# Kernel tuning notes

Measured on AMD Instinct MI355X. Metric: run time of the kernel, lower is better.

Reference implementation:

```python
import jax, jax.numpy as jnp
import numpy as np
import math

N_ENTITIES = 200000
N_ITEMS = 100000
N_REL = 40
DIM = 64
N_HEADS = 2
DK = DIM // N_HEADS
N_EDGES = 1500000
K_EDGES = 256
K_ITEMS = 100


def setup_inputs() -> dict:
    key = jax.random.key(0)
    k1, k2, k3, k4, k5, k6 = jax.random.split(key, 6)
    entity_emb = jax.random.normal(k1, (N_ENTITIES, DIM), jnp.float32) * 0.1
    W_Q = jax.random.normal(k2, (DIM, DIM), jnp.float32) * (1.0 / math.sqrt(DIM))
    relation_emb = jax.random.normal(k3, (N_REL - 1, DIM), jnp.float32) * 0.1
    edge_index = jax.random.randint(k4, (2, N_EDGES), 0, N_ENTITIES, jnp.int32)
    # edge_type in [1, N_REL-1]: code indexes relation_emb[edge_type - 1]
    edge_type = jax.random.randint(k5, (N_EDGES,), 1, N_REL, jnp.int32)
    # uniform(0,1) driving the gumbel noise -log(-log(u)); clipped away from 0
    noise_u = jax.random.uniform(k6, (N_EDGES,), jnp.float32, 1e-9, 1.0)
    return {"entity_emb": entity_emb, "W_Q": W_Q, "relation_emb": relation_emb,
            "noise_u": noise_u, "edge_index": edge_index, "edge_type": edge_type}


def reference(entity_emb, W_Q, relation_emb, noise_u, edge_index, edge_type):
    head, tail = edge_index[0], edge_index[1]
    E = edge_index.shape[1]

    # --- norm_attn_computer (AttnHGCN): per-edge multi-head attention ---
    # project once on nodes, then gather (same math as (emb[head] @ W_Q))
    proj = entity_emb @ W_Q                               # [N, D]
    q = proj[head].reshape(E, N_HEADS, DK)                # [E, H, Dk]
    k = proj[tail].reshape(E, N_HEADS, DK)                # [E, H, Dk]
    rel = relation_emb[edge_type - 1].reshape(E, N_HEADS, DK)
    attn = jnp.sum(q * k * rel, axis=-1) / math.sqrt(DK)  # [E, H]
    edge_attn_logits = attn.mean(axis=-1)                 # [E]

    # scatter_softmax over head nodes, then multiply by head degree (norm)
    seg_max = jax.lax.stop_gradient(
        jax.ops.segment_max(edge_attn_logits, head, num_segments=N_ENTITIES))
    ex = jnp.exp(edge_attn_logits - seg_max[head])
    denom = jax.ops.segment_sum(ex, head, num_segments=N_ENTITIES)
    edge_attn_score = ex / denom[head]
    deg = jax.ops.segment_sum(jnp.ones_like(edge_attn_logits), head,
                              num_segments=N_ENTITIES)
    edge_attn_score = edge_attn_score * deg[head]         # [E]

    # --- attn logit sums per item (head + tail scatter_sum), topk 100 ---
    sum_by_node = (jax.ops.segment_sum(edge_attn_logits, head, num_segments=N_ENTITIES)
                   + jax.ops.segment_sum(edge_attn_logits, tail, num_segments=N_ENTITIES))
    top_items_v, top_attn_items = jax.lax.top_k(sum_by_node[:N_ITEMS], K_ITEMS)

    # --- gumbel-noise injection + edge topk 256 ---
    noisy_score = edge_attn_score + (-jnp.log(-jnp.log(noise_u)))
    topk_v, topk_attn_edge_id = jax.lax.top_k(noisy_score, K_EDGES)

    return (edge_attn_score, topk_v, topk_attn_edge_id, top_items_v, top_attn_items)
```

## Files before the change

kernel.cpp:

```cpp
#include <hip/hip_runtime.h>

#define N_ENTITIES 200000
#define N_ITEMS    100000
#define DIM        64
#define N_EDGES    1500000
#define K_EDGES    256
#define K_ITEMS    100
#define SCALE      0.08838834764831845f

#define CAND_CAP   4096
#define NSCANB     ((N_ENTITIES + 255) / 256)

typedef unsigned long long u64;

__device__ __forceinline__ unsigned fkey(float x) {
    unsigned u = __float_as_uint(x);
    return (u & 0x80000000u) ? ~u : (u | 0x80000000u);
}
__device__ __forceinline__ float funkey(unsigned k) {
    return (k & 0x80000000u) ? __uint_as_float(k & 0x7fffffffu)
                             : __uint_as_float(~k);
}

__device__ __forceinline__ void lds_hist_add(unsigned* h, unsigned bin, bool valid, int lane) {
    bool need = valid;
    for (;;) {
        unsigned long long mask = __ballot(need);
        if (mask == 0ull) break;
        int leader = __ffsll(mask) - 1;
        unsigned lbin = __shfl(bin, leader, 64);
        bool same = need && (bin == lbin);
        unsigned long long grp = __ballot(same);
        if (lane == leader) atomicAdd(&h[lbin], (unsigned)__popcll(grp));
        need = need && !same;
    }
}

__device__ __forceinline__ unsigned select_digit(const unsigned* __restrict__ hist,
                                                 unsigned Keff, unsigned* above) {
    unsigned cum = 0;
    int b = 255;
    for (; b > 0; --b) {
        unsigned hb = hist[b];
        if (cum + hb >= Keff) break;
        cum += hb;
    }
    *above = cum;
    return (unsigned)b;
}

__global__ __launch_bounds__(256) void proj_kernel(const float* __restrict__ emb,
                                                   const float* __restrict__ W,
                                                   float* __restrict__ proj,
                                                   const int* __restrict__ head,
                                                   unsigned* __restrict__ degi,
                                                   unsigned* __restrict__ rank) {
    int e = blockIdx.x * blockDim.x + threadIdx.x;
    if (e < N_EDGES) rank[e] = atomicAdd(&degi[head[e]], 1u);

    __shared__ float part[4][16][64];
    const int t = threadIdx.x;
    const int c = t & 63;
    const int q = __builtin_amdgcn_readfirstlane(t >> 6);

    float Wreg[16];
#pragma unroll
    for (int j = 0; j < 16; ++j) Wreg[j] = W[(q * 16 + j) * 64 + c];

    const int base = blockIdx.x * 16;
    const float* erow = emb + (size_t)base * 64 + q * 16;

    float acc[16];
#pragma unroll
    for (int r = 0; r < 16; ++r) acc[r] = 0.f;
#pragma unroll
    for (int r = 0; r < 16; ++r) {
#pragma unroll
        for (int j = 0; j < 16; ++j)
            acc[r] += erow[r * 64 + j] * Wreg[j];
    }
#pragma unroll
    for (int r = 0; r < 16; ++r) part[q][r][c] = acc[r];
    __syncthreads();
#pragma unroll
    for (int it = 0; it < 4; ++it) {
        int oi = t + it * 256;
        int r = oi >> 6, cc = oi & 63;
        float s = part[0][r][cc] + part[1][r][cc] + part[2][r][cc] + part[3][r][cc];
        proj[(size_t)(base + r) * 64 + cc] = s;
    }
}

__global__ void scan1_kernel(const unsigned* __restrict__ degi, unsigned* __restrict__ start,
                             unsigned* __restrict__ bsum) {
    __shared__ unsigned s[256];
    int t = threadIdx.x, i = blockIdx.x * 256 + t;
    unsigned v = (i < N_ENTITIES) ? degi[i] : 0u;
    s[t] = v;
    __syncthreads();
    for (int off = 1; off < 256; off <<= 1) {
        unsigned x = s[t];
        unsigned y = (t >= off) ? s[t - off] : 0u;
        __syncthreads();
        s[t] = x + y;
        __syncthreads();
    }
    if (i < N_ENTITIES) start[i] = s[t] - v;
    if (t == 255) bsum[blockIdx.x] = s[t];
}

__global__ __launch_bounds__(256) void scan23_kernel(const unsigned* __restrict__ bsum,
                                                     unsigned* __restrict__ start) {
    __shared__ unsigned part[4];
    const int b = blockIdx.x;
    const int t = threadIdx.x;
    unsigned s = 0;
    for (int j = t; j < b; j += 256) s += bsum[j];
#pragma unroll
    for (int off = 1; off < 64; off <<= 1) s += __shfl_xor(s, off, 64);
    if ((t & 63) == 0) part[t >> 6] = s;
    __syncthreads();
    unsigned prefix = part[0] + part[1] + part[2] + part[3];
    int i = b * 256 + t;
    if (i < N_ENTITIES) start[i] += prefix;
}

__global__ void scatter_kernel(const int* __restrict__ head, const int* __restrict__ tail,
                               const int* __restrict__ etype,
                               const unsigned* __restrict__ rank,
                               const unsigned* __restrict__ start,
                               u64* __restrict__ rec) {
    int i = blockIdx.x * blockDim.x + threadIdx.x;
    if (i >= N_EDGES) return;
    unsigned slot = start[head[i]] + rank[i];
    u64 R = ((u64)(unsigned)tail[i] << 27) | ((u64)(unsigned)(etype[i] - 1) << 21) | (u64)(unsigned)i;
    rec[slot] = R;
}

__global__ __launch_bounds__(256) void node_pass(const float4* __restrict__ proj4,
                                                 const float4* __restrict__ rel4,
                                                 const u64* __restrict__ rec,
                                                 const unsigned* __restrict__ start,
                                                 const unsigned* __restrict__ degi,
                                                 float* __restrict__ logits,
                                                 float2* __restrict__ nd,
                                                 float* __restrict__ sumhead,
                                                 float* __restrict__ sumtail) {
    int wave = (blockIdx.x * blockDim.x + threadIdx.x) >> 6;
    int lane = threadIdx.x & 63;
    int slot = lane >> 4, sl = lane & 15;
    unsigned s = start[wave], len = degi[wave];
    float4 ph = proj4[(size_t)wave * 16 + sl];
    float dsum = 0.f, lsum = 0.f;
    for (unsigned k0 = 0; k0 < len; k0 += 8) {
        unsigned ka = k0 + slot, kb = ka + 4;
        bool va = (ka < len), vb = (kb < len);
        u64 Ra = rec[s + (va ? ka : 0u)];
        u64 Rb = rec[s + (vb ? kb : 0u)];
        unsigned ta = (unsigned)(Ra >> 27), ra = ((unsigned)(Ra >> 21)) & 63u;
        unsigned tb = (unsigned)(Rb >> 27), rb = ((unsigned)(Rb >> 21)) & 63u;
        unsigned ea = (unsigned)Ra & 0x1FFFFFu, eb = (unsigned)Rb & 0x1FFFFFu;
        float4 pa = proj4[(size_t)ta * 16 + sl];
        float4 qa = rel4[(size_t)ra * 16 + sl];
        float4 pb = proj4[(size_t)tb * 16 + sl];
        float4 qb = rel4[(size_t)rb * 16 + sl];
        float xa = ph.x * pa.x * qa.x + ph.y * pa.y * qa.y + ph.z * pa.z * qa.z + ph.w * pa.w * qa.w;
        float xb = ph.x * pb.x * qb.x + ph.y * pb.y * qb.y + ph.z * pb.z * qb.z + ph.w * pb.w * qb.w;
        xa += __shfl_xor(xa, 1, 64);  xb += __shfl_xor(xb, 1, 64);
        xa += __shfl_xor(xa, 2, 64);  xb += __shfl_xor(xb, 2, 64);
        xa += __shfl_xor(xa, 4, 64);  xb += __shfl_xor(xb, 4, 64);
        xa += __shfl_xor(xa, 8, 64);  xb += __shfl_xor(xb, 8, 64);
        if (sl == 0) {
            if (va) {
                float lg = xa * SCALE;
                logits[ea] = lg;
                dsum += __expf(lg);
                lsum += lg;
                if (ta < N_ITEMS) atomicAdd(&sumtail[ta], lg);
            }
            if (vb) {
                float lg = xb * SCALE;
                logits[eb] = lg;
                dsum += __expf(lg);
                lsum += lg;
                if (tb < N_ITEMS) atomicAdd(&sumtail[tb], lg);
            }
        }
    }
    dsum += __shfl_xor(dsum, 16, 64);
    dsum += __shfl_xor(dsum, 32, 64);
    lsum += __shfl_xor(lsum, 16, 64);
    lsum += __shfl_xor(lsum, 32, 64);
    if (lane == 0) {
        nd[wave] = make_float2(dsum, (float)len);
        sumhead[wave] = lsum;
    }
}

__global__ void edge_pass3(const float* __restrict__ logits, const int* __restrict__ head,
                           const float2* __restrict__ nd, const float* __restrict__ noise_u,
                           const float* __restrict__ sumhead, const float* __restrict__ sumtail,
                           float* __restrict__ out_scores, unsigned* __restrict__ keysE,
                           unsigned* __restrict__ keysI, unsigned* __restrict__ hists) {
    __shared__ unsigned hE[256];
    __shared__ unsigned hI[256];
    for (int j = threadIdx.x; j < 256; j += blockDim.x) { hE[j] = 0; hI[j] = 0; }
    __syncthreads();
    int i = blockIdx.x * blockDim.x + threadIdx.x;
    int lane = threadIdx.x & 63;

    unsigned bin = 0;
    bool valid = (i < N_EDGES);
    if (valid) {
        float lg = logits[i];
        float2 dd = nd[head[i]];
        float score = __expf(lg) / dd.x * dd.y;
        out_scores[i] = score;
        float noise = -logf(-logf(noise_u[i]));
        unsigned k = fkey(score + noise);
        keysE[i] = k;
        bin = k >> 24;
    }
    lds_hist_add(hE, bin, valid, lane);

    bin = 0;
    valid = (i < N_ITEMS);
    if (valid) {
        float s = sumhead[i] + sumtail[i];
        unsigned k = fkey(s);
        keysI[i] = k;
        bin = k >> 24;
    }
    lds_hist_add(hI, bin, valid, lane);

    __syncthreads();
    for (int j = threadIdx.x; j < 256; j += blockDim.x) {
        unsigned v = hE[j];
        if (v) atomicAdd(&hists[j], v);
        v = hI[j];
        if (v) atomicAdd(&hists[3 * 256 + j], v);
    }
}

__global__ void hist_stage_kernel(const unsigned* __restrict__ keysE,
                                  const unsigned* __restrict__ keysI,
                                  unsigned* __restrict__ hists, int stage) {
    __shared__ unsigned h[256];
    for (int j = threadIdx.x; j < 256; j += blockDim.x) h[j] = 0;
    __syncthreads();
    const int y = blockIdx.y;
    const unsigned* keys = y ? keysI : keysE;
    const int n = y ? N_ITEMS : N_EDGES;
    const unsigned K = y ? K_ITEMS : K_EDGES;
    unsigned* H = hists + (size_t)y * 3 * 256;

    unsigned aboveA, prefix;
    unsigned binA = select_digit(H, K, &aboveA);
    if (stage == 1) {
        prefix = binA;
    } else {
        unsigned aboveB;
        unsigned binB = select_digit(H + 256, K - aboveA, &aboveB);
        prefix = (binA << 8) | binB;
    }
    const int shift = 24 - 8 * stage;
    unsigned* out = H + stage * 256;

    const int lane = threadIdx.x & 63;
    const int stride = gridDim.x * blockDim.x;
    for (int idx = blockIdx.x * blockDim.x + threadIdx.x; idx - lane < n; idx += stride) {
        bool valid = (idx < n);
        unsigned bin = 0;
        if (valid) {
            unsigned k = keys[idx];
            if ((k >> (shift + 8)) != prefix) valid = false;
            bin = (k >> shift) & 0xFFu;
        }
        lds_hist_add(h, bin, valid, lane);
    }
    __syncthreads();
    for (int j = threadIdx.x; j < 256; j += blockDim.x) {
        unsigned v = h[j];
        if (v) atomicAdd(&out[j], v);
    }
}

__global__ void collect_kernel(const unsigned* __restrict__ keysE,
                               const unsigned* __restrict__ keysI,
                               const unsigned* __restrict__ hists,
                               unsigned* __restrict__ counters, unsigned* __restrict__ cand) {
    const int y = blockIdx.y;
    const unsigned* keys = y ? keysI : keysE;
    const int n = y ? N_ITEMS : N_EDGES;
    const unsigned K = y ? K_ITEMS : K_EDGES;
    const unsigned* H = hists + (size_t)y * 3 * 256;
    unsigned aboveA, aboveB, aboveC;
    unsigned binA = select_digit(H, K, &aboveA);
    unsigned binB = select_digit(H + 256, K - aboveA, &aboveB);
    unsigned binC = select_digit(H + 512, K - aboveA - aboveB, &aboveC);
    const unsigned T = ((binA << 16) | (binB << 8) | binC) << 8;
    unsigned* cd = cand + (size_t)y * 2 * CAND_CAP;

    int i = blockIdx.x * blockDim.x + threadIdx.x;
    int stride = gridDim.x * blockDim.x;
    for (; i < n; i += stride) {
        unsigned k = keys[i];
        if (k >= T) {
            unsigned p = atomicAdd(&counters[y], 1u);
            if (p < (unsigned)CAND_CAP) { cd[2 * p] = k; cd[2 * p + 1] = (unsigned)i; }
        }
    }
}

__global__ void final_topk_kernel(const unsigned* __restrict__ cand,
                                  const unsigned* __restrict__ counters,
                                  float* __restrict__ out_topkv, float* __restrict__ out_topki,
                                  float* __restrict__ out_itemv, float* __restrict__ out_itemi) {
    __shared__ unsigned sk[CAND_CAP];
    __shared__ unsigned si[CAND_CAP];
    const int y = blockIdx.x;
    const int K = y ? K_ITEMS : K_EDGES;
    float* outv = y ? out_itemv : out_topkv;
    float* outi = y ? out_itemi : out_topki;
    const unsigned* cd = cand + (size_t)y * 2 * CAND_CAP;
    unsigned m = counters[y];
    if (m > (unsigned)CAND_CAP) m = CAND_CAP;
    for (unsigned i = threadIdx.x; i < m; i += blockDim.x) {
        sk[i] = cd[2 * i];
        si[i] = cd[2 * i + 1];
    }
    __syncthreads();
    for (unsigned i = threadIdx.x; i < m; i += blockDim.x) {
        unsigned ki = sk[i], xi = si[i];
        int r = 0;
        for (unsigned j = 0; j < m; ++j) {
            unsigned kj = sk[j];
            if (kj > ki || (kj == ki && si[j] < xi)) r++;
        }
        if (r < K) {
            outv[r] = funkey(ki);
            outi[r] = (float)xi;
        }
    }
}

extern "C" void kernel_launch(void* const* d_in, const int* in_sizes, int n_in,
                              void* d_out, int out_size, void* d_ws, size_t ws_size,
                              hipStream_t stream) {
    (void)in_sizes; (void)n_in; (void)out_size; (void)ws_size;
    const float* emb    = (const float*)d_in[0];
    const float* W      = (const float*)d_in[1];
    const float* rel    = (const float*)d_in[2];
    const float* noise  = (const float*)d_in[3];
    const int*   eidx   = (const int*)d_in[4];
    const int*   etype  = (const int*)d_in[5];
    const int* head = eidx;
    const int* tail = eidx + N_EDGES;

    float* out        = (float*)d_out;
    float* out_scores = out;
    float* out_topkv  = out + N_EDGES;
    float* out_topki  = out + N_EDGES + K_EDGES;
    float* out_itemv  = out + N_EDGES + 2 * K_EDGES;
    float* out_itemi  = out + N_EDGES + 2 * K_EDGES + K_ITEMS;

    float* ws = (float*)d_ws;
    size_t o = 0;
    float*    proj    = ws + o;               o += (size_t)N_ENTITIES * DIM;
    unsigned* rank    = (unsigned*)(ws + o);
    float*    logits  = ws + o;               o += N_EDGES;
    u64*      rec     = (u64*)(ws + o);       o += 2 * (size_t)N_EDGES;
    unsigned* keysE   = (unsigned*)rec;
    unsigned* keysI   = keysE + N_EDGES;
    unsigned* start   = (unsigned*)(ws + o);  o += N_ENTITIES;
    unsigned* degi    = (unsigned*)(ws + o);  o += N_ENTITIES;
    float*    sumtail = ws + o;               o += N_ITEMS;
    unsigned* hists   = (unsigned*)(ws + o);  o += 2 * 3 * 256;
    unsigned* counters= (unsigned*)(ws + o);  o += 2;
    float2*   nd      = (float2*)(ws + o);    o += 2 * (size_t)N_ENTITIES;
    float*    sumhead = ws + o;               o += N_ENTITIES;
    unsigned* bsum    = (unsigned*)(ws + o);  o += 1024;
    unsigned* cand    = (unsigned*)(ws + o);  o += 2 * 2 * CAND_CAP;

    hipMemsetAsync(degi, 0, (size_t)(N_ENTITIES + N_ITEMS + 2 * 3 * 256 + 2) * 4, stream);
    hipLaunchKernelGGL(proj_kernel, dim3(12500), dim3(256), 0, stream,
                       emb, W, proj, head, degi, rank);
    hipLaunchKernelGGL(scan1_kernel, dim3(NSCANB), dim3(256), 0, stream, degi, start, bsum);
    hipLaunchKernelGGL(scan23_kernel, dim3(NSCANB), dim3(256), 0, stream, bsum, start);
    hipLaunchKernelGGL(scatter_kernel, dim3((N_EDGES + 255) / 256), dim3(256), 0, stream,
                       head, tail, etype, rank, start, rec);
    hipLaunchKernelGGL(node_pass, dim3(N_ENTITIES / 4), dim3(256), 0, stream,
                       (const float4*)proj, (const float4*)rel, rec, start, degi,
                       logits, nd, sumhead, sumtail);
    hipLaunchKernelGGL(edge_pass3, dim3((N_EDGES + 255) / 256), dim3(256), 0, stream,
                       logits, head, (const float2*)nd, noise, sumhead, sumtail,
                       out_scores, keysE, keysI, hists);
    hipLaunchKernelGGL(hist_stage_kernel, dim3(512, 2), dim3(256), 0, stream,
                       keysE, keysI, hists, 1);
    hipLaunchKernelGGL(hist_stage_kernel, dim3(512, 2), dim3(256), 0, stream,
                       keysE, keysI, hists, 2);
    hipLaunchKernelGGL(collect_kernel, dim3(512, 2), dim3(256), 0, stream,
                       keysE, keysI, hists, counters, cand);
    hipLaunchKernelGGL(final_topk_kernel, dim3(2), dim3(1024), 0, stream,
                       cand, counters, out_topkv, out_topki, out_itemv, out_itemi);
}
```

Baseline: 502.3 us.

## Replicate tail-sum accumulators per XCD and defer rank store in projection

```diff
diff --git a/kernel.cpp b/kernel.cpp
--- a/kernel.cpp
+++ b/kernel.cpp
@@ -56,7 +56,9 @@
                                                    unsigned* __restrict__ degi,
                                                    unsigned* __restrict__ rank) {
     int e = blockIdx.x * blockDim.x + threadIdx.x;
-    if (e < N_EDGES) rank[e] = atomicAdd(&degi[head[e]], 1u);
+    unsigned rk = 0;
+    bool haveEdge = (e < N_EDGES);
+    if (haveEdge) rk = atomicAdd(&degi[head[e]], 1u);
 
     __shared__ float part[4][16][64];
     const int t = threadIdx.x;
@@ -89,6 +91,7 @@
         float s = part[0][r][cc] + part[1][r][cc] + part[2][r][cc] + part[3][r][cc];
         proj[(size_t)(base + r) * 64 + cc] = s;
     }
+    if (haveEdge) rank[e] = rk;
 }
 
 __global__ void scan1_kernel(const unsigned* __restrict__ degi, unsigned* __restrict__ start,
@@ -145,7 +148,12 @@
                                                  float* __restrict__ logits,
                                                  float2* __restrict__ nd,
                                                  float* __restrict__ sumhead,
-                                                 float* __restrict__ sumtail) {
+                                                 float* __restrict__ sumtailR,
+                                                 int repMask) {
+    unsigned xcd;
+    asm volatile("s_getreg_b32 %0, hwreg(HW_REG_XCC_ID)" : "=s"(xcd));
+    float* st = sumtailR + (size_t)(xcd & (unsigned)repMask) * N_ITEMS;
+
     int wave = (blockIdx.x * blockDim.x + threadIdx.x) >> 6;
     int lane = threadIdx.x & 63;
     int slot = lane >> 4, sl = lane & 15;
@@ -176,14 +184,14 @@
                 logits[ea] = lg;
                 dsum += __expf(lg);
                 lsum += lg;
-                if (ta < N_ITEMS) atomicAdd(&sumtail[ta], lg);
+                if (ta < N_ITEMS) atomicAdd(&st[ta], lg);
             }
             if (vb) {
                 float lg = xb * SCALE;
                 logits[eb] = lg;
                 dsum += __expf(lg);
                 lsum += lg;
-                if (tb < N_ITEMS) atomicAdd(&sumtail[tb], lg);
+                if (tb < N_ITEMS) atomicAdd(&st[tb], lg);
             }
         }
     }
@@ -199,7 +207,8 @@
 
 __global__ void edge_pass3(const float* __restrict__ logits, const int* __restrict__ head,
                            const float2* __restrict__ nd, const float* __restrict__ noise_u,
-                           const float* __restrict__ sumhead, const float* __restrict__ sumtail,
+                           const float* __restrict__ sumhead, const float* __restrict__ sumtailR,
+                           int R,
                            float* __restrict__ out_scores, unsigned* __restrict__ keysE,
                            unsigned* __restrict__ keysI, unsigned* __restrict__ hists) {
     __shared__ unsigned hE[256];
@@ -226,7 +235,8 @@
     bin = 0;
     valid = (i < N_ITEMS);
     if (valid) {
-        float s = sumhead[i] + sumtail[i];
+        float s = sumhead[i];
+        for (int r = 0; r < R; ++r) s += sumtailR[(size_t)r * N_ITEMS + i];
         unsigned k = fkey(s);
         keysI[i] = k;
         bin = k >> 24;
@@ -347,7 +357,7 @@
 extern "C" void kernel_launch(void* const* d_in, const int* in_sizes, int n_in,
                               void* d_out, int out_size, void* d_ws, size_t ws_size,
                               hipStream_t stream) {
-    (void)in_sizes; (void)n_in; (void)out_size; (void)ws_size;
+    (void)in_sizes; (void)n_in; (void)out_size;
     const float* emb    = (const float*)d_in[0];
     const float* W      = (const float*)d_in[1];
     const float* rel    = (const float*)d_in[2];
@@ -363,6 +373,15 @@
     float* out_topki  = out + N_EDGES + K_EDGES;
     float* out_itemv  = out + N_EDGES + 2 * K_EDGES;
     float* out_itemi  = out + N_EDGES + 2 * K_EDGES + K_ITEMS;
+
+    auto layout_floats = [](int R) -> size_t {
+        return (size_t)N_ENTITIES * DIM + N_EDGES + 2 * (size_t)N_EDGES
+             + N_ENTITIES + N_ENTITIES + (size_t)R * N_ITEMS
+             + 2 * 3 * 256 + 2 + 2 * (size_t)N_ENTITIES + N_ENTITIES
+             + 1024 + 2 * 2 * CAND_CAP;
+    };
+    int R = 8;
+    while (R > 1 && ws_size < layout_floats(R) * 4) R >>= 1;
 
     float* ws = (float*)d_ws;
     size_t o = 0;
@@ -374,7 +393,7 @@
     unsigned* keysI   = keysE + N_EDGES;
     unsigned* start   = (unsigned*)(ws + o);  o += N_ENTITIES;
     unsigned* degi    = (unsigned*)(ws + o);  o += N_ENTITIES;
-    float*    sumtail = ws + o;               o += N_ITEMS;
+    float*    sumtailR= ws + o;               o += (size_t)R * N_ITEMS;
     unsigned* hists   = (unsigned*)(ws + o);  o += 2 * 3 * 256;
     unsigned* counters= (unsigned*)(ws + o);  o += 2;
     float2*   nd      = (float2*)(ws + o);    o += 2 * (size_t)N_ENTITIES;
@@ -382,7 +401,8 @@
     unsigned* bsum    = (unsigned*)(ws + o);  o += 1024;
     unsigned* cand    = (unsigned*)(ws + o);  o += 2 * 2 * CAND_CAP;
 
-    hipMemsetAsync(degi, 0, (size_t)(N_ENTITIES + N_ITEMS + 2 * 3 * 256 + 2) * 4, stream);
+    hipMemsetAsync(degi, 0,
+                   ((size_t)N_ENTITIES + (size_t)R * N_ITEMS + 2 * 3 * 256 + 2) * 4, stream);
     hipLaunchKernelGGL(proj_kernel, dim3(12500), dim3(256), 0, stream,
                        emb, W, proj, head, degi, rank);
     hipLaunchKernelGGL(scan1_kernel, dim3(NSCANB), dim3(256), 0, stream, degi, start, bsum);
@@ -391,9 +411,9 @@
                        head, tail, etype, rank, start, rec);
     hipLaunchKernelGGL(node_pass, dim3(N_ENTITIES / 4), dim3(256), 0, stream,
                        (const float4*)proj, (const float4*)rel, rec, start, degi,
-                       logits, nd, sumhead, sumtail);
+                       logits, nd, sumhead, sumtailR, R - 1);
     hipLaunchKernelGGL(edge_pass3, dim3((N_EDGES + 255) / 256), dim3(256), 0, stream,
-                       logits, head, (const float2*)nd, noise, sumhead, sumtail,
+                       logits, head, (const float2*)nd, noise, sumhead, sumtailR, R,
                        out_scores, keysE, keysI, hists);
     hipLaunchKernelGGL(hist_stage_kernel, dim3(512, 2), dim3(256), 0, stream,
                        keysE, keysI, hists, 1);
```

New measurement: 498.8 us. About the same (-0.7%).

## Fuse edge scoring into node pass and replicate atomic counters per XCC

Applied to the files above, without the earlier changes.

```diff
diff --git a/kernel.cpp b/kernel.cpp
--- a/kernel.cpp
+++ b/kernel.cpp
@@ -10,6 +10,7 @@
 
 #define CAND_CAP   4096
 #define NSCANB     ((N_ENTITIES + 255) / 256)
+#define CAP        128
 
 typedef unsigned long long u64;
 
@@ -20,6 +21,12 @@
 __device__ __forceinline__ float funkey(unsigned k) {
     return (k & 0x80000000u) ? __uint_as_float(k & 0x7fffffffu)
                              : __uint_as_float(~k);
+}
+
+__device__ __forceinline__ unsigned xcc_id() {
+    unsigned x;
+    asm volatile("s_getreg_b32 %0, hwreg(HW_REG_XCC_ID)" : "=s"(x));
+    return x;
 }
 
 __device__ __forceinline__ void lds_hist_add(unsigned* h, unsigned bin, bool valid, int lane) {
@@ -49,15 +56,18 @@
     return (unsigned)b;
 }
 
+__global__ void count_kernel(const int* __restrict__ head,
+                             unsigned* __restrict__ degiR, unsigned* __restrict__ rank) {
+    int e = blockIdx.x * blockDim.x + threadIdx.x;
+    if (e >= N_EDGES) return;
+    unsigned rep = xcc_id() & 1u;
+    unsigned old = atomicAdd(&degiR[rep * N_ENTITIES + head[e]], 1u);
+    rank[e] = (rep << 31) | old;
+}
+
 __global__ __launch_bounds__(256) void proj_kernel(const float* __restrict__ emb,
                                                    const float* __restrict__ W,
-                                                   float* __restrict__ proj,
-                                                   const int* __restrict__ head,
-                                                   unsigned* __restrict__ degi,
-                                                   unsigned* __restrict__ rank) {
-    int e = blockIdx.x * blockDim.x + threadIdx.x;
-    if (e < N_EDGES) rank[e] = atomicAdd(&degi[head[e]], 1u);
-
+                                                   float* __restrict__ proj) {
     __shared__ float part[4][16][64];
     const int t = threadIdx.x;
     const int c = t & 63;
@@ -91,11 +101,11 @@
     }
 }
 
-__global__ void scan1_kernel(const unsigned* __restrict__ degi, unsigned* __restrict__ start,
+__global__ void scan1_kernel(const unsigned* __restrict__ degiR, unsigned* __restrict__ start,
                              unsigned* __restrict__ bsum) {
     __shared__ unsigned s[256];
     int t = threadIdx.x, i = blockIdx.x * 256 + t;
-    unsigned v = (i < N_ENTITIES) ? degi[i] : 0u;
+    unsigned v = (i < N_ENTITIES) ? (degiR[i] + degiR[N_ENTITIES + i]) : 0u;
     s[t] = v;
     __syncthreads();
     for (int off = 1; off < 256; off <<= 1) {
@@ -129,10 +139,13 @@
                                const int* __restrict__ etype,
                                const unsigned* __restrict__ rank,
                                const unsigned* __restrict__ start,
+                               const unsigned* __restrict__ degiR,
                                u64* __restrict__ rec) {
     int i = blockIdx.x * blockDim.x + threadIdx.x;
     if (i >= N_EDGES) return;
-    unsigned slot = start[head[i]] + rank[i];
+    int h = head[i];
+    unsigned rk = rank[i];
+    unsigned slot = start[h] + ((rk >> 31) ? degiR[h] : 0u) + (rk & 0x7FFFFFFFu);
     u64 R = ((u64)(unsigned)tail[i] << 27) | ((u64)(unsigned)(etype[i] - 1) << 21) | (u64)(unsigned)i;
     rec[slot] = R;
 }
@@ -141,17 +154,29 @@
                                                  const float4* __restrict__ rel4,
                                                  const u64* __restrict__ rec,
                                                  const unsigned* __restrict__ start,
-                                                 const unsigned* __restrict__ degi,
-                                                 float* __restrict__ logits,
-                                                 float2* __restrict__ nd,
+                                                 const float* __restrict__ noise_u,
+                                                 float* __restrict__ out_scores,
+                                                 unsigned* __restrict__ keysE,
                                                  float* __restrict__ sumhead,
-                                                 float* __restrict__ sumtail) {
-    int wave = (blockIdx.x * blockDim.x + threadIdx.x) >> 6;
+                                                 float* __restrict__ sumtailR,
+                                                 unsigned* __restrict__ histE) {
+    __shared__ float ex[4][CAP];
+    __shared__ unsigned hE[256];
+    hE[threadIdx.x] = 0;
+    __syncthreads();
+
+    float* strep = sumtailR + (size_t)(xcc_id() & 1u) * N_ITEMS;
+
+    int node = (blockIdx.x * blockDim.x + threadIdx.x) >> 6;
+    int w = threadIdx.x >> 6;
     int lane = threadIdx.x & 63;
     int slot = lane >> 4, sl = lane & 15;
-    unsigned s = start[wave], len = degi[wave];
-    float4 ph = proj4[(size_t)wave * 16 + sl];
+    unsigned s = start[node];
+    unsigned e1 = (node + 1 < N_ENTITIES) ? start[node + 1] : (unsigned)N_EDGES;
+    unsigned len = e1 - s;
+    float4 ph = proj4[(size_t)node * 16 + sl];
     float dsum = 0.f, lsum = 0.f;
+
     for (unsigned k0 = 0; k0 < len; k0 += 8) {
         unsigned ka = k0 + slot, kb = ka + 4;
         bool va = (ka < len), vb = (kb < len);
@@ -159,7 +184,6 @@
         u64 Rb = rec[s + (vb ? kb : 0u)];
         unsigned ta = (unsigned)(Ra >> 27), ra = ((unsigned)(Ra >> 21)) & 63u;
         unsigned tb = (unsigned)(Rb >> 27), rb = ((unsigned)(Rb >> 21)) & 63u;
-        unsigned ea = (unsigned)Ra & 0x1FFFFFu, eb = (unsigned)Rb & 0x1FFFFFu;
         float4 pa = proj4[(size_t)ta * 16 + sl];
         float4 qa = rel4[(size_t)ra * 16 + sl];
         float4 pb = proj4[(size_t)tb * 16 + sl];
@@ -173,17 +197,19 @@
         if (sl == 0) {
             if (va) {
                 float lg = xa * SCALE;
-                logits[ea] = lg;
-                dsum += __expf(lg);
+                float E = __expf(lg);
+                if (ka < CAP) ex[w][ka] = E;
+                dsum += E;
                 lsum += lg;
-                if (ta < N_ITEMS) atomicAdd(&sumtail[ta], lg);
+                if (ta < N_ITEMS) atomicAdd(&strep[ta], lg);
             }
             if (vb) {
                 float lg = xb * SCALE;
-                logits[eb] = lg;
-                dsum += __expf(lg);
+                float E = __expf(lg);
+                if (kb < CAP) ex[w][kb] = E;
+                dsum += E;
                 lsum += lg;
-                if (tb < N_ITEMS) atomicAdd(&sumtail[tb], lg);
+                if (tb < N_ITEMS) atomicAdd(&strep[tb], lg);
             }
         }
     }
@@ -191,55 +217,52 @@
     dsum += __shfl_xor(dsum, 32, 64);
     lsum += __shfl_xor(lsum, 16, 64);
     lsum += __shfl_xor(lsum, 32, 64);
-    if (lane == 0) {
-        nd[wave] = make_float2(dsum, (float)len);
-        sumhead[wave] = lsum;
-    }
-}
-
-__global__ void edge_pass3(const float* __restrict__ logits, const int* __restrict__ head,
-                           const float2* __restrict__ nd, const float* __restrict__ noise_u,
-                           const float* __restrict__ sumhead, const float* __restrict__ sumtail,
-                           float* __restrict__ out_scores, unsigned* __restrict__ keysE,
-                           unsigned* __restrict__ keysI, unsigned* __restrict__ hists) {
-    __shared__ unsigned hE[256];
-    __shared__ unsigned hI[256];
-    for (int j = threadIdx.x; j < 256; j += blockDim.x) { hE[j] = 0; hI[j] = 0; }
+    dsum = __shfl(dsum, 0, 64);
+    if (lane == 0) sumhead[node] = lsum;
+    float flen = (float)len;
+    __syncthreads();
+
+    for (unsigned k0 = 0; k0 < len; k0 += 64) {
+        unsigned k = k0 + lane;
+        bool valid = (k < len);
+        unsigned bin = 0;
+        if (valid) {
+            u64 R = rec[s + k];
+            unsigned eid = (unsigned)R & 0x1FFFFFu;
+            float E = ex[w][k < CAP ? k : CAP - 1];
+            float score = E / dsum * flen;
+            float nu = noise_u[eid];
+            unsigned kk = fkey(score - logf(-logf(nu)));
+            out_scores[eid] = score;
+            keysE[eid] = kk;
+            bin = kk >> 24;
+        }
+        lds_hist_add(hE, bin, valid, lane);
+    }
+    __syncthreads();
+    unsigned v = hE[threadIdx.x];
+    if (v) atomicAdd(&histE[threadIdx.x], v);
+}
+
+__global__ void item_kernel(const float* __restrict__ sumhead, const float* __restrict__ sumtailR,
+                            unsigned* __restrict__ keysI, unsigned* __restrict__ histI) {
+    __shared__ unsigned h[256];
+    h[threadIdx.x] = 0;
     __syncthreads();
     int i = blockIdx.x * blockDim.x + threadIdx.x;
     int lane = threadIdx.x & 63;
-
     unsigned bin = 0;
-    bool valid = (i < N_EDGES);
+    bool valid = (i < N_ITEMS);
     if (valid) {
-        float lg = logits[i];
-        float2 dd = nd[head[i]];
-        float score = __expf(lg) / dd.x * dd.y;
-        out_scores[i] = score;
-        float noise = -logf(-logf(noise_u[i]));
-        unsigned k = fkey(score + noise);
-        keysE[i] = k;
-        bin = k >> 24;
-    }
-    lds_hist_add(hE, bin, valid, lane);
-
-    bin = 0;
-    valid = (i < N_ITEMS);
-    if (valid) {
-        float s = sumhead[i] + sumtail[i];
+        float s = sumhead[i] + sumtailR[i] + sumtailR[N_ITEMS + i];
         unsigned k = fkey(s);
         keysI[i] = k;
         bin = k >> 24;
     }
-    lds_hist_add(hI, bin, valid, lane);
-
-    __syncthreads();
-    for (int j = threadIdx.x; j < 256; j += blockDim.x) {
-        unsigned v = hE[j];
-        if (v) atomicAdd(&hists[j], v);
-        v = hI[j];
-        if (v) atomicAdd(&hists[3 * 256 + j], v);
-    }
+    lds_hist_add(h, bin, valid, lane);
+    __syncthreads();
+    unsigned v = h[threadIdx.x];
+    if (v) atomicAdd(&histI[threadIdx.x], v);
 }
 
 __global__ void hist_stage_kernel(const unsigned* __restrict__ keysE,
@@ -368,33 +391,32 @@
     size_t o = 0;
     float*    proj    = ws + o;               o += (size_t)N_ENTITIES * DIM;
     unsigned* rank    = (unsigned*)(ws + o);
-    float*    logits  = ws + o;               o += N_EDGES;
-    u64*      rec     = (u64*)(ws + o);       o += 2 * (size_t)N_EDGES;
-    unsigned* keysE   = (unsigned*)rec;
-    unsigned* keysI   = keysE + N_EDGES;
+    unsigned* keysE   = (unsigned*)(ws + o);  o += N_EDGES;
+    u64*      rec     = (u64*)(ws + o);
+    unsigned* keysI   = (unsigned*)rec;       o += 2 * (size_t)N_EDGES;
     unsigned* start   = (unsigned*)(ws + o);  o += N_ENTITIES;
-    unsigned* degi    = (unsigned*)(ws + o);  o += N_ENTITIES;
-    float*    sumtail = ws + o;               o += N_ITEMS;
+    unsigned* degiR   = (unsigned*)(ws + o);  o += 2 * (size_t)N_ENTITIES;
+    float*    sumtailR= (float*)degiR;
     unsigned* hists   = (unsigned*)(ws + o);  o += 2 * 3 * 256;
     unsigned* counters= (unsigned*)(ws + o);  o += 2;
-    float2*   nd      = (float2*)(ws + o);    o += 2 * (size_t)N_ENTITIES;
     float*    sumhead = ws + o;               o += N_ENTITIES;
     unsigned* bsum    = (unsigned*)(ws + o);  o += 1024;
     unsigned* cand    = (unsigned*)(ws + o);  o += 2 * 2 * CAND_CAP;
 
-    hipMemsetAsync(degi, 0, (size_t)(N_ENTITIES + N_ITEMS + 2 * 3 * 256 + 2) * 4, stream);
-    hipLaunchKernelGGL(proj_kernel, dim3(12500), dim3(256), 0, stream,
-                       emb, W, proj, head, degi, rank);
-    hipLaunchKernelGGL(scan1_kernel, dim3(NSCANB), dim3(256), 0, stream, degi, start, bsum);
+    hipMemsetAsync(degiR, 0, (2 * (size_t)N_ENTITIES + 2 * 3 * 256 + 2) * 4, stream);
+    hipLaunchKernelGGL(count_kernel, dim3((N_EDGES + 255) / 256), dim3(256), 0, stream,
+                       head, degiR, rank);
+    hipLaunchKernelGGL(proj_kernel, dim3(12500), dim3(256), 0, stream, emb, W, proj);
+    hipLaunchKernelGGL(scan1_kernel, dim3(NSCANB), dim3(256), 0, stream, degiR, start, bsum);
     hipLaunchKernelGGL(scan23_kernel, dim3(NSCANB), dim3(256), 0, stream, bsum, start);
     hipLaunchKernelGGL(scatter_kernel, dim3((N_EDGES + 255) / 256), dim3(256), 0, stream,
-                       head, tail, etype, rank, start, rec);
+                       head, tail, etype, rank, start, degiR, rec);
+    hipMemsetAsync(sumtailR, 0, 2 * (size_t)N_ITEMS * 4, stream);
     hipLaunchKernelGGL(node_pass, dim3(N_ENTITIES / 4), dim3(256), 0, stream,
-                       (const float4*)proj, (const float4*)rel, rec, start, degi,
-                       logits, nd, sumhead, sumtail);
-    hipLaunchKernelGGL(edge_pass3, dim3((N_EDGES + 255) / 256), dim3(256), 0, stream,
-                       logits, head, (const float2*)nd, noise, sumhead, sumtail,
-                       out_scores, keysE, keysI, hists);
+                       (const float4*)proj, (const float4*)rel, rec, start, noise,
+                       out_scores, keysE, sumhead, sumtailR, hists);
+    hipLaunchKernelGGL(item_kernel, dim3((N_ITEMS + 255) / 256), dim3(256), 0, stream,
+                       sumhead, sumtailR, keysI, hists + 3 * 256);
     hipLaunchKernelGGL(hist_stage_kernel, dim3(512, 2), dim3(256), 0, stream,
                        keysE, keysI, hists, 1);
     hipLaunchKernelGGL(hist_stage_kernel, dim3(512, 2), dim3(256), 0, stream,
```

Result: slower. 990.4 us (+97.2%).
